# Kernel tuning notes

Measured on AMD Instinct MI355X. Metric: run time of the kernel, lower is better.

The kernel has to match this reference:

```python
import jax, jax.numpy as jnp
import numpy as np

N = 100000
LEAKY_SLOPE = 0.2


def gat_conv(x, W, att_src, att_dst, b, src, dst, num_nodes):
    """PyG-style GATConv (concat=True). x:[N,Fin], W:[Fin,H*C], att_*:[1,H,C], b:[H*C]."""
    H, C = att_src.shape[1], att_src.shape[2]
    h = (x @ W).reshape(num_nodes, H, C)                      # [N,H,C]
    a_src = jnp.sum(h * att_src, axis=-1)                     # [N,H]
    a_dst = jnp.sum(h * att_dst, axis=-1)                     # [N,H]
    e = jax.nn.leaky_relu(a_src[src] + a_dst[dst], LEAKY_SLOPE)  # [E,H]
    # segment softmax over destination neighborhoods
    m = jax.ops.segment_max(e, dst, num_segments=num_nodes)   # [N,H]
    m = jnp.where(jnp.isfinite(m), m, 0.0)
    ex = jnp.exp(e - m[dst])                                  # [E,H]
    s = jax.ops.segment_sum(ex, dst, num_segments=num_nodes)  # [N,H]
    alpha = ex / (s[dst] + 1e-16)                             # [E,H]
    msg = h[src] * alpha[:, :, None]                          # [E,H,C]
    out = jax.ops.segment_sum(msg, dst, num_segments=num_nodes)  # [N,H,C]
    return out.reshape(num_nodes, H * C) + b


def setup_inputs() -> dict:
    key = jax.random.key(0)
    ks = jax.random.split(key, 8)
    F_in, H, C, n_cls = 256, 4, 32, 16
    E = 1_600_000
    x = jax.random.normal(ks[0], (N, F_in), dtype=jnp.float32)
    edge_index = jax.random.randint(ks[1], (2, E), 0, N, dtype=jnp.int64)
    sc1 = 1.0 / np.sqrt(F_in)
    sc2 = 1.0 / np.sqrt(H * C)
    return {
        "x": x,
        "edge_index": edge_index,
        "W1": jax.random.normal(ks[2], (F_in, H * C), dtype=jnp.float32) * sc1,
        "att_src1": jax.random.normal(ks[3], (1, H, C), dtype=jnp.float32) * sc2,
        "att_dst1": jax.random.normal(ks[4], (1, H, C), dtype=jnp.float32) * sc2,
        "b1": jnp.zeros((H * C,), dtype=jnp.float32),
        "W2": jax.random.normal(ks[5], (H * C, n_cls), dtype=jnp.float32) * sc2,
        "att_src2": jax.random.normal(ks[6], (1, 1, n_cls), dtype=jnp.float32) * 0.25,
        "att_dst2": jax.random.normal(ks[7], (1, 1, n_cls), dtype=jnp.float32) * 0.25,
        "b2": jnp.zeros((n_cls,), dtype=jnp.float32),
    }


def reference(x, edge_index, W1, att_src1, att_dst1, b1, W2, att_src2, att_dst2, b2):
    # add self-loops (PyG GATConv default)
    loop = jnp.arange(N, dtype=edge_index.dtype)
    src = jnp.concatenate([edge_index[0], loop])
    dst = jnp.concatenate([edge_index[1], loop])
    # eval mode: dropout(p=0.6) is identity
    h = gat_conv(x, W1, att_src1, att_dst1, b1, src, dst, N)
    h = jax.nn.elu(h)
    out = gat_conv(h, W2, att_src2, att_dst2, b2, src, dst, N)
    return out
```

## Files before the change

kernel.cpp:

```cpp
#include <hip/hip_runtime.h>
#include <hip/hip_fp16.h>
#include <cfloat>
#include <cmath>

#define LEAKY 0.2f

typedef _Float16 half8 __attribute__((ext_vector_type(8)));
typedef float f32x4 __attribute__((ext_vector_type(4)));

__device__ __forceinline__ void edge_sd(const int* __restrict__ ei, int e, int E, int& s, int& d) {
    if (e < E) { s = ei[e]; d = ei[E + e]; }
    else       { s = e - E; d = e - E; }
}

__device__ __forceinline__ int wave_incl_scan(int x, int lane) {
#pragma unroll
    for (int off = 1; off < 64; off <<= 1) {
        int y = __shfl_up(x, off);
        if (lane >= off) x += y;
    }
    return x;
}

__global__ __launch_bounds__(1024) void scan_blk_k(const int* __restrict__ cnt,
                                                   int* __restrict__ rowptr,
                                                   int* __restrict__ part, int Nn) {
    __shared__ int wsum[16];
    const int t = threadIdx.x, lane = t & 63, w = t >> 6;
    const int i = blockIdx.x * 1024 + t;
    int v = (i < Nn) ? cnt[i] : 0;
    int sc = wave_incl_scan(v, lane);
    if (lane == 63) wsum[w] = sc;
    __syncthreads();
    if (w == 0 && lane < 16) {
        int x = wsum[lane];
#pragma unroll
        for (int off = 1; off < 16; off <<= 1) {
            int y = __shfl_up(x, off);
            if (lane >= off) x += y;
        }
        wsum[lane] = x;
    }
    __syncthreads();
    int excl = sc - v + (w ? wsum[w - 1] : 0);
    if (i < Nn) rowptr[i] = excl;
    if (t == 1023) part[blockIdx.x] = wsum[15];
}

__global__ __launch_bounds__(128) void scan_part_k(int* __restrict__ part, int nb) {
    __shared__ int sm[128];
    int t = threadIdx.x;
    int v = (t < nb) ? part[t] : 0;
    sm[t] = v; __syncthreads();
    for (int off = 1; off < 128; off <<= 1) {
        int add = (t >= off) ? sm[t - off] : 0;
        __syncthreads();
        sm[t] += add;
        __syncthreads();
    }
    if (t < nb) part[t] = sm[t] - v;
}

__global__ __launch_bounds__(1024) void scan_add_k(int* __restrict__ rowptr,
                                                   const int* __restrict__ part,
                                                   int Nn, int ET) {
    int i = blockIdx.x * 1024 + threadIdx.x;
    if (i < Nn) rowptr[i] += part[blockIdx.x];
    if (i == 0) rowptr[Nn] = ET;
}

__global__ void scatter_k(const int* __restrict__ ei, int E, int Nn,
                          const int* __restrict__ rowptr, const int* __restrict__ rank,
                          int* __restrict__ srcs) {
    const int E4 = E >> 2;
    int tid = blockIdx.x * 256 + threadIdx.x;
    if (tid < E4) {
        int4 s4 = *(const int4*)&ei[tid * 4];
        int4 d4 = *(const int4*)&ei[E + tid * 4];
        int4 r4 = *(const int4*)&rank[tid * 4];
        srcs[rowptr[d4.x] + r4.x] = s4.x;
        srcs[rowptr[d4.y] + r4.y] = s4.y;
        srcs[rowptr[d4.z] + r4.z] = s4.z;
        srcs[rowptr[d4.w] + r4.w] = s4.w;
    } else {
        int i = tid - E4;
        if (i < Nn) srcs[rowptr[i] + rank[E + i]] = i;
    }
}

__global__ void wpack1_k(const float* __restrict__ W1, _Float16* __restrict__ Wpk) {
    int g = blockIdx.x * 256 + threadIdx.x;
    if (g >= 4096) return;
    int t = g >> 9, s = (g >> 6) & 7, l = g & 63;
    int krow = s * 32 + ((l >> 4) << 3);
    int col = t * 16 + (l & 15);
    half8 v;
#pragma unroll
    for (int j = 0; j < 8; ++j) v[j] = (_Float16)W1[(size_t)(krow + j) * 128 + col];
    *(half8*)&Wpk[(size_t)g * 8] = v;
}

#define GEMM_BLOCKS 1024
__global__ __launch_bounds__(512) void fat_k(const int* __restrict__ ei, int E, int Nn,
                                             int* __restrict__ cnt, int* __restrict__ rank,
                                             int nBuildF,
                                             const float* __restrict__ x,
                                             const _Float16* __restrict__ Wpk,
                                             const float* __restrict__ att_s,
                                             const float* __restrict__ att_d,
                                             _Float16* __restrict__ h1,
                                             float* __restrict__ a1s,
                                             float* __restrict__ a1d, int Mt) {
    __shared__ __align__(16) _Float16 xs[32 * 256];
    const int t = threadIdx.x;

    if ((int)blockIdx.x < nBuildF) {
        const int E4 = E >> 2;
        int tid = blockIdx.x * 512 + t;
        if (tid < E4) {
            int4 d4 = *(const int4*)&ei[E + tid * 4];
            int4 r;
            r.x = atomicAdd(&cnt[d4.x], 1);
            r.y = atomicAdd(&cnt[d4.y], 1);
            r.z = atomicAdd(&cnt[d4.z], 1);
            r.w = atomicAdd(&cnt[d4.w], 1);
            *(int4*)&rank[tid * 4] = r;
        } else {
            int i = tid - E4;
            if (i < Nn) rank[E + i] = atomicAdd(&cnt[i], 1);
        }
        return;
    }

    const int gb = blockIdx.x - nBuildF;
    const int l = t & 63;
    const int w = t >> 6;
    const int mstr = w >> 2;
    const int npair = w & 3;

    half8 bf0[8], bf1[8];
#pragma unroll
    for (int s = 0; s < 8; ++s) {
        bf0[s] = *(const half8*)&Wpk[(size_t)(((npair * 2 + 0) * 8 + s) * 64 + l) * 8];
        bf1[s] = *(const half8*)&Wpk[(size_t)(((npair * 2 + 1) * 8 + s) * 64 + l) * 8];
    }
    const float as0 = att_s[npair * 32 + (l & 15)];
    const float as1 = att_s[npair * 32 + 16 + (l & 15)];
    const float ad0 = att_d[npair * 32 + (l & 15)];
    const float ad1 = att_d[npair * 32 + 16 + (l & 15)];

    const int r = t >> 4;
    const int kc = t & 15;
    const int swz = (r & 7) << 4;
    const int arow = mstr * 16 + (l & 15);
    const int aswz = (arow & 7) << 4;
    const int abase = arow * 256;

    for (int mt = gb; mt < Mt; mt += GEMM_BLOCKS) {
        const int mBase = mt * 32;
        const float4* xrow = (const float4*)(x + (size_t)(mBase + r) * 256);
#pragma unroll
        for (int i = 0; i < 4; ++i) {
            float4 v = xrow[kc + i * 16];
            union { _Float16 h[4]; uint2 u; } cv;
            cv.h[0] = (_Float16)v.x; cv.h[1] = (_Float16)v.y;
            cv.h[2] = (_Float16)v.z; cv.h[3] = (_Float16)v.w;
            int kb = kc * 8 + i * 128;
            *(uint2*)&xs[r * 256 + ((kb ^ swz) >> 1)] = cv.u;
        }
        __syncthreads();
        f32x4 acc0 = {0.f, 0.f, 0.f, 0.f}, acc1 = {0.f, 0.f, 0.f, 0.f};
#pragma unroll
        for (int s = 0; s < 8; ++s) {
            int kb = s * 64 + ((l >> 4) << 4);
            half8 a = *(const half8*)&xs[abase + ((kb ^ aswz) >> 1)];
            acc0 = __builtin_amdgcn_mfma_f32_16x16x32_f16(a, bf0[s], acc0, 0, 0, 0);
            acc1 = __builtin_amdgcn_mfma_f32_16x16x32_f16(a, bf1[s], acc1, 0, 0, 0);
        }
        const int drow = mBase + mstr * 16 + ((l >> 4) << 2);
        const int dcol = npair * 32 + (l & 15);
#pragma unroll
        for (int rr = 0; rr < 4; ++rr) {
            h1[(size_t)(drow + rr) * 128 + dcol]      = (_Float16)acc0[rr];
            h1[(size_t)(drow + rr) * 128 + dcol + 16] = (_Float16)acc1[rr];
            float ps = acc0[rr] * as0 + acc1[rr] * as1;
            float pd = acc0[rr] * ad0 + acc1[rr] * ad1;
#pragma unroll
            for (int off = 1; off < 16; off <<= 1) {
                ps += __shfl_xor(ps, off);
                pd += __shfl_xor(pd, off);
            }
            if ((l & 15) == 0) {
                a1s[(drow + rr) * 4 + npair] = ps;
                a1d[(drow + rr) * 4 + npair] = pd;
            }
        }
        __syncthreads();
    }
}

__global__ __launch_bounds__(256) void agg1_k(const int* __restrict__ rowptr,
                                              const int* __restrict__ srcs,
                                              const float* __restrict__ a1s,
                                              const float* __restrict__ a1d,
                                              const __half* __restrict__ h1,
                                              const float* __restrict__ b1,
                                              const float* __restrict__ W2,
                                              const float* __restrict__ att_s2,
                                              const float* __restrict__ att_d2,
                                              __half* __restrict__ h2,
                                              float* __restrict__ a2s,
                                              float* __restrict__ a2d, int Nn) {
    __shared__ int   s_s[4][64];
    __shared__ float s_al[4][64][4];
    __shared__ float rowb[4][128];
    __shared__ float w2s[128 * 16];
    const int wv = threadIdx.x >> 6;
    const int lane = threadIdx.x & 63;
    const int n = blockIdx.x * 4 + wv;

    for (int i4 = threadIdx.x; i4 < 512; i4 += 256)
        *(float4*)&w2s[i4 * 4] = *(const float4*)&W2[i4 * 4];

    if (n < Nn) {
        const int beg = rowptr[n], end = rowptr[n + 1];
        const int cnt = end - beg;
        const float4 ad4 = ((const float4*)a1d)[n];

        int e = beg + lane;
        bool val = e < end;
        int sv = val ? srcs[e] : 0;
        float4 a = ((const float4*)a1s)[sv];
        float v0 = a.x + ad4.x, v1 = a.y + ad4.y, v2 = a.z + ad4.z, v3 = a.w + ad4.w;
        v0 = fmaxf(v0, LEAKY * v0); v1 = fmaxf(v1, LEAKY * v1);
        v2 = fmaxf(v2, LEAKY * v2); v3 = fmaxf(v3, LEAKY * v3);
        float al0 = val ? __expf(v0) : 0.0f, al1 = val ? __expf(v1) : 0.0f;
        float al2 = val ? __expf(v2) : 0.0f, al3 = val ? __expf(v3) : 0.0f;
        float t0 = al0, t1 = al1, t2 = al2, t3 = al3;
        for (int base = beg + 64; base < end; base += 64) {
            int ee = base + lane; bool vv = ee < end;
            int ss = vv ? srcs[ee] : 0;
            float4 aa = ((const float4*)a1s)[ss];
            float w0 = aa.x + ad4.x, w1 = aa.y + ad4.y, w2v = aa.z + ad4.z, w3 = aa.w + ad4.w;
            w0 = fmaxf(w0, LEAKY * w0); w1 = fmaxf(w1, LEAKY * w1);
            w2v = fmaxf(w2v, LEAKY * w2v); w3 = fmaxf(w3, LEAKY * w3);
            if (vv) { t0 += __expf(w0); t1 += __expf(w1); t2 += __expf(w2v); t3 += __expf(w3); }
        }
#pragma unroll
        for (int off = 1; off < 64; off <<= 1) {
            t0 += __shfl_xor(t0, off); t1 += __shfl_xor(t1, off);
            t2 += __shfl_xor(t2, off); t3 += __shfl_xor(t3, off);
        }
        const float i0 = 1.0f / (t0 + 1e-16f), i1 = 1.0f / (t1 + 1e-16f);
        const float i2 = 1.0f / (t2 + 1e-16f), i3 = 1.0f / (t3 + 1e-16f);

        const int hc = lane >> 4;
        float2 acc = make_float2(0.0f, 0.0f);
        const size_t lo = 2 * lane;

        s_s[wv][lane] = sv;
        s_al[wv][lane][0] = al0 * i0; s_al[wv][lane][1] = al1 * i1;
        s_al[wv][lane][2] = al2 * i2; s_al[wv][lane][3] = al3 * i3;
        int wcnt = cnt < 64 ? cnt : 64;
        int ko = 0;
        for (; ko + 4 <= wcnt; ko += 4) {
            int s0 = s_s[wv][ko+0], s1 = s_s[wv][ko+1];
            int s2 = s_s[wv][ko+2], s3 = s_s[wv][ko+3];
            float p0 = s_al[wv][ko+0][hc], p1 = s_al[wv][ko+1][hc];
            float p2 = s_al[wv][ko+2][hc], p3 = s_al[wv][ko+3][hc];
            float2 g0 = __half22float2(*(const __half2*)&h1[(size_t)s0 * 128 + lo]);
            float2 g1 = __half22float2(*(const __half2*)&h1[(size_t)s1 * 128 + lo]);
            float2 g2 = __half22float2(*(const __half2*)&h1[(size_t)s2 * 128 + lo]);
            float2 g3 = __half22float2(*(const __half2*)&h1[(size_t)s3 * 128 + lo]);
            acc.x = fmaf(p0, g0.x, acc.x); acc.y = fmaf(p0, g0.y, acc.y);
            acc.x = fmaf(p1, g1.x, acc.x); acc.y = fmaf(p1, g1.y, acc.y);
            acc.x = fmaf(p2, g2.x, acc.x); acc.y = fmaf(p2, g2.y, acc.y);
            acc.x = fmaf(p3, g3.x, acc.x); acc.y = fmaf(p3, g3.y, acc.y);
        }
        for (; ko < wcnt; ++ko) {
            int s = s_s[wv][ko];
            float p = s_al[wv][ko][hc];
            float2 g = __half22float2(*(const __half2*)&h1[(size_t)s * 128 + lo]);
            acc.x = fmaf(p, g.x, acc.x); acc.y = fmaf(p, g.y, acc.y);
        }
        for (int base = beg + 64; base < end; base += 64) {
            int ee = base + lane; bool vv = ee < end;
            int ss = vv ? srcs[ee] : 0;
            float4 aa = ((const float4*)a1s)[ss];
            float w0 = aa.x + ad4.x, w1 = aa.y + ad4.y, w2v = aa.z + ad4.z, w3 = aa.w + ad4.w;
            w0 = fmaxf(w0, LEAKY * w0); w1 = fmaxf(w1, LEAKY * w1);
            w2v = fmaxf(w2v, LEAKY * w2v); w3 = fmaxf(w3, LEAKY * w3);
            s_s[wv][lane] = ss;
            s_al[wv][lane][0] = vv ? __expf(w0) * i0 : 0.0f;
            s_al[wv][lane][1] = vv ? __expf(w1) * i1 : 0.0f;
            s_al[wv][lane][2] = vv ? __expf(w2v) * i2 : 0.0f;
            s_al[wv][lane][3] = vv ? __expf(w3) * i3 : 0.0f;
            int wc = end - base; if (wc > 64) wc = 64;
            for (int k2 = 0; k2 < wc; ++k2) {
                int s = s_s[wv][k2];
                float p = s_al[wv][k2][hc];
                float2 g = __half22float2(*(const __half2*)&h1[(size_t)s * 128 + lo]);
                acc.x = fmaf(p, g.x, acc.x); acc.y = fmaf(p, g.y, acc.y);
            }
        }
        float2 bb = *(const float2*)&b1[2 * lane];
        float ox = acc.x + bb.x, oy = acc.y + bb.y;
        ox = ox > 0.0f ? ox : expm1f(ox);
        oy = oy > 0.0f ? oy : expm1f(oy);
        rowb[wv][2 * lane] = ox;
        rowb[wv][2 * lane + 1] = oy;
    }
    __syncthreads();
    if (n >= Nn) return;

    const int q = lane >> 4, j = lane & 15;
    const float* rb = rowb[wv];
    float part = 0.0f;
#pragma unroll
    for (int kk = 0; kk < 32; ++kk) {
        int k = kk * 4 + q;
        part = fmaf(rb[k], w2s[k * 16 + j], part);
    }
    part += __shfl_xor(part, 16);
    part += __shfl_xor(part, 32);
    float vs = part * att_s2[j];
    float vd = part * att_d2[j];
#pragma unroll
    for (int off = 1; off < 16; off <<= 1) {
        vs += __shfl_xor(vs, off);
        vd += __shfl_xor(vd, off);
    }
    if (lane < 16) h2[(size_t)n * 16 + j] = __float2half(part);
    if (lane == 0) { a2s[n] = vs; a2d[n] = vd; }
}

__global__ __launch_bounds__(256) void agg2_k(const int* __restrict__ rowptr,
                                              const int* __restrict__ srcs,
                                              const float* __restrict__ a2s,
                                              const float* __restrict__ a2d,
                                              const __half* __restrict__ h2,
                                              const float* __restrict__ b2,
                                              float* __restrict__ dout, int Nn) {
    __shared__ int   s_s[4][64];
    __shared__ float s_al[4][64];
    const int wv = threadIdx.x >> 6;
    const int lane = threadIdx.x & 63;
    const int n = blockIdx.x * 4 + wv;
    if (n >= Nn) return;
    const int beg = rowptr[n], end = rowptr[n + 1];
    const int cnt = end - beg;
    const float adn = a2d[n];

    int e = beg + lane;
    bool val = e < end;
    int sv = val ? srcs[e] : 0;
    float av = a2s[sv] + adn;
    av = fmaxf(av, LEAKY * av);
    float al = val ? __expf(av) : 0.0f;
    float ss = al;
    for (int base = beg + 64; base < end; base += 64) {
        int ee = base + lane; bool vv = ee < end;
        float aw = a2s[vv ? srcs[ee] : 0] + adn;
        aw = fmaxf(aw, LEAKY * aw);
        if (vv) ss += __expf(aw);
    }
#pragma unroll
    for (int off = 1; off < 64; off <<= 1) ss += __shfl_xor(ss, off);
    const float sinv = 1.0f / (ss + 1e-16f);

    const int eg = lane >> 4, j = lane & 15;
    float acc = 0.0f;
    s_s[wv][lane] = sv;
    s_al[wv][lane] = al * sinv;
    int wcnt = cnt < 64 ? cnt : 64;
    int ko = eg;
    for (; ko + 4 < wcnt; ko += 8) {
        int s0 = s_s[wv][ko], s1 = s_s[wv][ko + 4];
        float p0 = s_al[wv][ko], p1 = s_al[wv][ko + 4];
        float g0 = __half2float(h2[(size_t)s0 * 16 + j]);
        float g1 = __half2float(h2[(size_t)s1 * 16 + j]);
        acc = fmaf(p0, g0, acc);
        acc = fmaf(p1, g1, acc);
    }
    for (; ko < wcnt; ko += 4) {
        acc = fmaf(s_al[wv][ko], __half2float(h2[(size_t)s_s[wv][ko] * 16 + j]), acc);
    }
    for (int base = beg + 64; base < end; base += 64) {
        int ee = base + lane; bool vv = ee < end;
        int sn = vv ? srcs[ee] : 0;
        float aw = a2s[sn] + adn;
        aw = fmaxf(aw, LEAKY * aw);
        s_s[wv][lane] = sn;
        s_al[wv][lane] = vv ? __expf(aw) * sinv : 0.0f;
        int wc = end - base; if (wc > 64) wc = 64;
        for (int k2 = eg; k2 < wc; k2 += 4) {
            acc = fmaf(s_al[wv][k2], __half2float(h2[(size_t)s_s[wv][k2] * 16 + j]), acc);
        }
    }
    acc += __shfl_xor(acc, 16);
    acc += __shfl_xor(acc, 32);
    if (lane < 16) dout[(size_t)n * 16 + j] = acc + b2[j];
}

extern "C" void kernel_launch(void* const* d_in, const int* in_sizes, int n_in,
                              void* d_out, int out_size, void* d_ws, size_t ws_size,
                              hipStream_t stream) {
    const float* x      = (const float*)d_in[0];
    const int*   ei     = (const int*)d_in[1];
    const float* W1     = (const float*)d_in[2];
    const float* att_s1 = (const float*)d_in[3];
    const float* att_d1 = (const float*)d_in[4];
    const float* b1     = (const float*)d_in[5];
    const float* W2     = (const float*)d_in[6];
    const float* att_s2 = (const float*)d_in[7];
    const float* att_d2 = (const float*)d_in[8];
    const float* b2     = (const float*)d_in[9];
    float* dout = (float*)d_out;

    const int Nn = in_sizes[0] / 256;
    const int E  = in_sizes[1] / 2;
    const int ET = E + Nn;

    char* p = (char*)d_ws;
    auto alloc = [&](size_t bytes) { char* r = p; p += (bytes + 255) & ~(size_t)255; return r; };
    _Float16* h1  = (_Float16*)alloc((size_t)Nn * 128 * 2);
    __half* h2    = (__half*)alloc((size_t)Nn * 16 * 2);
    _Float16* Wpk = (_Float16*)alloc(4096 * 8 * 2);
    float* a1s    = (float*)alloc((size_t)Nn * 4 * 4);
    float* a1d    = (float*)alloc((size_t)Nn * 4 * 4);
    float* a2s    = (float*)alloc((size_t)Nn * 4);
    float* a2d    = (float*)alloc((size_t)Nn * 4);
    int* rowptr   = (int*)alloc((size_t)(Nn + 1) * 4);
    int* cnt      = (int*)alloc((size_t)Nn * 4);
    int* rank     = (int*)alloc((size_t)ET * 4);
    int* part     = (int*)alloc(128 * 4);
    int* srcs     = (int*)alloc((size_t)ET * 4);

    const int nbScan = (Nn + 1023) / 1024;
    const int nBuildF = (E / 4 + Nn + 511) / 512;
    const int nBuild256 = (E / 4 + Nn + 255) / 256;

    hipMemsetAsync(cnt, 0, (size_t)Nn * 4, stream);
    wpack1_k<<<dim3(16), dim3(256), 0, stream>>>(W1, Wpk);
    fat_k<<<dim3(nBuildF + GEMM_BLOCKS), dim3(512), 0, stream>>>(
        ei, E, Nn, cnt, rank, nBuildF,
        x, Wpk, att_s1, att_d1, h1, a1s, a1d, Nn / 32);
    scan_blk_k<<<dim3(nbScan), dim3(1024), 0, stream>>>(cnt, rowptr, part, Nn);
    scan_part_k<<<dim3(1), dim3(128), 0, stream>>>(part, nbScan);
    scan_add_k<<<dim3(nbScan), dim3(1024), 0, stream>>>(rowptr, part, Nn, ET);
    scatter_k<<<dim3(nBuild256), dim3(256), 0, stream>>>(ei, E, Nn, rowptr, rank, srcs);
    agg1_k<<<dim3((Nn + 3) / 4), dim3(256), 0, stream>>>(rowptr, srcs, a1s, a1d,
                                                         (const __half*)h1, b1,
                                                         W2, att_s2, att_d2,
                                                         h2, a2s, a2d, Nn);
    agg2_k<<<dim3((Nn + 3) / 4), dim3(256), 0, stream>>>(rowptr, srcs, a2s, a2d, h2, b2, dout, Nn);
}
```

Measured before the change: 277.9 us.

## Map four nodes per wave in agg2 and fold the partial scan into the add

agg2 now assigns a 16-lane group to each destination node, so one wave handles four nodes instead of one. With an average degree near 17, the old one-node-per-wave layout left most of its 64 lanes idle. The scan_part kernel is also removed: each add block reduces the preceding block partials itself, saving one launch at the cost of a small redundant reduction per block. Lanes in a wave can now diverge when their nodes have different degrees, and nodes with more than 16 edges take several 16-edge passes.

```diff
diff --git a/kernel.cpp b/kernel.cpp
--- a/kernel.cpp
+++ b/kernel.cpp
@@ -7,11 +7,6 @@
 
 typedef _Float16 half8 __attribute__((ext_vector_type(8)));
 typedef float f32x4 __attribute__((ext_vector_type(4)));
-
-__device__ __forceinline__ void edge_sd(const int* __restrict__ ei, int e, int E, int& s, int& d) {
-    if (e < E) { s = ei[e]; d = ei[E + e]; }
-    else       { s = e - E; d = e - E; }
-}
 
 __device__ __forceinline__ int wave_incl_scan(int x, int lane) {
 #pragma unroll
@@ -47,25 +42,21 @@
     if (t == 1023) part[blockIdx.x] = wsum[15];
 }
 
-__global__ __launch_bounds__(128) void scan_part_k(int* __restrict__ part, int nb) {
-    __shared__ int sm[128];
-    int t = threadIdx.x;
-    int v = (t < nb) ? part[t] : 0;
-    sm[t] = v; __syncthreads();
-    for (int off = 1; off < 128; off <<= 1) {
-        int add = (t >= off) ? sm[t - off] : 0;
-        __syncthreads();
-        sm[t] += add;
-        __syncthreads();
-    }
-    if (t < nb) part[t] = sm[t] - v;
-}
-
-__global__ __launch_bounds__(1024) void scan_add_k(int* __restrict__ rowptr,
-                                                   const int* __restrict__ part,
-                                                   int Nn, int ET) {
-    int i = blockIdx.x * 1024 + threadIdx.x;
-    if (i < Nn) rowptr[i] += part[blockIdx.x];
+__global__ __launch_bounds__(1024) void scan_add2_k(int* __restrict__ rowptr,
+                                                    const int* __restrict__ part,
+                                                    int Nn, int ET) {
+    __shared__ int sprefix;
+    const int t = threadIdx.x;
+    if (t < 64) {
+        int x = 0;
+        for (int i = t; i < (int)blockIdx.x; i += 64) x += part[i];
+#pragma unroll
+        for (int off = 1; off < 64; off <<= 1) x += __shfl_xor(x, off);
+        if (t == 0) sprefix = x;
+    }
+    __syncthreads();
+    int i = blockIdx.x * 1024 + t;
+    if (i < Nn) rowptr[i] += sprefix;
     if (i == 0) rowptr[Nn] = ET;
 }
 
@@ -341,65 +332,71 @@
                                               const __half* __restrict__ h2,
                                               const float* __restrict__ b2,
                                               float* __restrict__ dout, int Nn) {
-    __shared__ int   s_s[4][64];
-    __shared__ float s_al[4][64];
+    __shared__ int   s_s[4][4][16];
+    __shared__ float s_al[4][4][16];
     const int wv = threadIdx.x >> 6;
     const int lane = threadIdx.x & 63;
-    const int n = blockIdx.x * 4 + wv;
+    const int g = lane >> 4;
+    const int j = lane & 15;
+    const int n = (blockIdx.x * 4 + wv) * 4 + g;
     if (n >= Nn) return;
     const int beg = rowptr[n], end = rowptr[n + 1];
     const int cnt = end - beg;
     const float adn = a2d[n];
 
-    int e = beg + lane;
+    int e = beg + j;
     bool val = e < end;
     int sv = val ? srcs[e] : 0;
     float av = a2s[sv] + adn;
     av = fmaxf(av, LEAKY * av);
     float al = val ? __expf(av) : 0.0f;
-    float ss = al;
-    for (int base = beg + 64; base < end; base += 64) {
-        int ee = base + lane; bool vv = ee < end;
+    float ssum = al;
+    for (int base = beg + 16; base < end; base += 16) {
+        int ee = base + j; bool vv = ee < end;
         float aw = a2s[vv ? srcs[ee] : 0] + adn;
         aw = fmaxf(aw, LEAKY * aw);
-        if (vv) ss += __expf(aw);
-    }
-#pragma unroll
-    for (int off = 1; off < 64; off <<= 1) ss += __shfl_xor(ss, off);
-    const float sinv = 1.0f / (ss + 1e-16f);
-
-    const int eg = lane >> 4, j = lane & 15;
+        if (vv) ssum += __expf(aw);
+    }
+#pragma unroll
+    for (int off = 1; off < 16; off <<= 1) ssum += __shfl_xor(ssum, off);
+    const float sinv = 1.0f / (ssum + 1e-16f);
+
+    s_s[wv][g][j] = sv;
+    s_al[wv][g][j] = al * sinv;
     float acc = 0.0f;
-    s_s[wv][lane] = sv;
-    s_al[wv][lane] = al * sinv;
-    int wcnt = cnt < 64 ? cnt : 64;
-    int ko = eg;
-    for (; ko + 4 < wcnt; ko += 8) {
-        int s0 = s_s[wv][ko], s1 = s_s[wv][ko + 4];
-        float p0 = s_al[wv][ko], p1 = s_al[wv][ko + 4];
+    int wcnt = cnt < 16 ? cnt : 16;
+    int ko = 0;
+    for (; ko + 2 <= wcnt; ko += 2) {
+        int s0 = s_s[wv][g][ko], s1 = s_s[wv][g][ko + 1];
+        float p0 = s_al[wv][g][ko], p1 = s_al[wv][g][ko + 1];
         float g0 = __half2float(h2[(size_t)s0 * 16 + j]);
         float g1 = __half2float(h2[(size_t)s1 * 16 + j]);
         acc = fmaf(p0, g0, acc);
         acc = fmaf(p1, g1, acc);
     }
-    for (; ko < wcnt; ko += 4) {
-        acc = fmaf(s_al[wv][ko], __half2float(h2[(size_t)s_s[wv][ko] * 16 + j]), acc);
-    }
-    for (int base = beg + 64; base < end; base += 64) {
-        int ee = base + lane; bool vv = ee < end;
+    if (ko < wcnt)
+        acc = fmaf(s_al[wv][g][ko], __half2float(h2[(size_t)s_s[wv][g][ko] * 16 + j]), acc);
+    for (int base = beg + 16; base < end; base += 16) {
+        int ee = base + j; bool vv = ee < end;
         int sn = vv ? srcs[ee] : 0;
         float aw = a2s[sn] + adn;
         aw = fmaxf(aw, LEAKY * aw);
-        s_s[wv][lane] = sn;
-        s_al[wv][lane] = vv ? __expf(aw) * sinv : 0.0f;
-        int wc = end - base; if (wc > 64) wc = 64;
-        for (int k2 = eg; k2 < wc; k2 += 4) {
-            acc = fmaf(s_al[wv][k2], __half2float(h2[(size_t)s_s[wv][k2] * 16 + j]), acc);
-        }
-    }
-    acc += __shfl_xor(acc, 16);
-    acc += __shfl_xor(acc, 32);
-    if (lane < 16) dout[(size_t)n * 16 + j] = acc + b2[j];
+        s_s[wv][g][j] = sn;
+        s_al[wv][g][j] = vv ? __expf(aw) * sinv : 0.0f;
+        int wc = end - base; if (wc > 16) wc = 16;
+        int k2 = 0;
+        for (; k2 + 2 <= wc; k2 += 2) {
+            int s0 = s_s[wv][g][k2], s1 = s_s[wv][g][k2 + 1];
+            float p0 = s_al[wv][g][k2], p1 = s_al[wv][g][k2 + 1];
+            float g0 = __half2float(h2[(size_t)s0 * 16 + j]);
+            float g1 = __half2float(h2[(size_t)s1 * 16 + j]);
+            acc = fmaf(p0, g0, acc);
+            acc = fmaf(p1, g1, acc);
+        }
+        if (k2 < wc)
+            acc = fmaf(s_al[wv][g][k2], __half2float(h2[(size_t)s_s[wv][g][k2] * 16 + j]), acc);
+    }
+    dout[(size_t)n * 16 + j] = acc + b2[j];
 }
 
 extern "C" void kernel_launch(void* const* d_in, const int* in_sizes, int n_in,
@@ -446,12 +443,11 @@
         ei, E, Nn, cnt, rank, nBuildF,
         x, Wpk, att_s1, att_d1, h1, a1s, a1d, Nn / 32);
     scan_blk_k<<<dim3(nbScan), dim3(1024), 0, stream>>>(cnt, rowptr, part, Nn);
-    scan_part_k<<<dim3(1), dim3(128), 0, stream>>>(part, nbScan);
-    scan_add_k<<<dim3(nbScan), dim3(1024), 0, stream>>>(rowptr, part, Nn, ET);
+    scan_add2_k<<<dim3(nbScan), dim3(1024), 0, stream>>>(rowptr, part, Nn, ET);
     scatter_k<<<dim3(nBuild256), dim3(256), 0, stream>>>(ei, E, Nn, rowptr, rank, srcs);
     agg1_k<<<dim3((Nn + 3) / 4), dim3(256), 0, stream>>>(rowptr, srcs, a1s, a1d,
                                                          (const __half*)h1, b1,
                                                          W2, att_s2, att_d2,
                                                          h2, a2s, a2d, Nn);
-    agg2_k<<<dim3((Nn + 3) / 4), dim3(256), 0, stream>>>(rowptr, srcs, a2s, a2d, h2, b2, dout, Nn);
-}
+    agg2_k<<<dim3((Nn + 15) / 16), dim3(256), 0, stream>>>(rowptr, srcs, a2s, a2d, h2, b2, dout, Nn);
+}
```

Measured after the change: 267.1 us, median of 2. 3.9% less time.
